# Kernel tuning notes

Measured on AMD Instinct MI355X. Metric: run time of the kernel, lower is better.

## Reference

```python
import jax, jax.numpy as jnp
import numpy as np

N_NODES = 100000
N_EDGES = 3200000
D_NODE = 5            # per-node feature dim
D_IN = 2 * D_NODE     # 10, MLP input dim
D_HID = D_IN * 5      # 50, HIDDEN_DIM_MULTIPLIER = 5


def setup_inputs() -> dict:
    key = jax.random.key(0)
    ks = jax.random.split(key, 8)
    x = jax.random.normal(ks[0], (N_NODES, D_NODE), dtype=jnp.float32)
    edge_index = jax.random.randint(ks[1], (2, N_EDGES), 0, N_NODES, dtype=jnp.int64)
    s1 = 1.0 / np.sqrt(D_IN)
    s2 = 1.0 / np.sqrt(D_HID)
    W1 = jax.random.uniform(ks[2], (D_IN, D_HID), jnp.float32, -s1, s1)
    b1 = jax.random.uniform(ks[3], (D_HID,), jnp.float32, -s1, s1)
    W2 = jax.random.uniform(ks[4], (D_HID, D_HID), jnp.float32, -s2, s2)
    b2 = jax.random.uniform(ks[5], (D_HID,), jnp.float32, -s2, s2)
    W3 = jax.random.uniform(ks[6], (D_HID, 1), jnp.float32, -s2, s2)
    b3 = jax.random.uniform(ks[7], (1,), jnp.float32, -s2, s2)
    return {"x": x, "edge_index": edge_index, "W1": W1, "b1": b1,
            "W2": W2, "b2": b2, "W3": W3, "b3": b3}


def reference(x, edge_index, W1, b1, W2, b2, W3, b3):
    # gather src/tgt node features and concat -> [E, 2*D_NODE]
    ef = jnp.concatenate([x[edge_index[0]], x[edge_index[1]]], axis=-1)
    h = jax.nn.relu(ef @ W1 + b1)
    h = jax.nn.relu(h @ W2 + b2)
    return jax.nn.sigmoid(h @ W3 + b3)  # [E, 1]
```

## Files before the change

### kernel.cpp

```cpp
#include <hip/hip_runtime.h>
#include <hip/hip_bf16.h>

typedef short bf16x8 __attribute__((ext_vector_type(8)));
typedef float f32x4  __attribute__((ext_vector_type(4)));

union fragU { f32x4 f; bf16x8 b; uint4 q; uint u[4]; };

__device__ inline ushort f2bf(float f) {
    union { float f; uint u; } v; v.f = f;
    uint r = (v.u + 0x7FFFu + ((v.u >> 16) & 1u)) >> 16;
    return (ushort)r;
}
__device__ inline uint packbf(float a, float b) {
    return (uint)f2bf(a) | ((uint)f2bf(b) << 16);
}
__device__ inline uint cvtpk(float lo, float hi) {
    uint r;
    asm("v_cvt_pk_bf16_f32 %0, %1, %2" : "=v"(r) : "v"(lo), "v"(hi));
    return r;
}

__global__ __launch_bounds__(256) void pack_x_kernel(
    const float* __restrict__ x, uint4* __restrict__ xp, int N)
{
    int i = blockIdx.x * blockDim.x + threadIdx.x;
    if (i > N) return;
    uint4 o = {0u, 0u, 0u, 0u};
    if (i < N) {
        const float* r = x + (size_t)i * 5;
        o.x = packbf(r[0], r[1]);
        o.y = packbf(r[2], r[3]);
        o.z = packbf(r[4], 1.0f);
    }
    xp[i] = o;
}

__global__ __launch_bounds__(64) void pack_w_kernel(
    const float* __restrict__ W1, const float* __restrict__ b1,
    const float* __restrict__ W2, const float* __restrict__ b2,
    const float* __restrict__ W3, uint4* __restrict__ tab)
{
    const int lane = threadIdx.x;
    const int c = lane & 15;
    const int g = lane >> 4;

    union { ushort s[8]; uint4 q; } u;
    #pragma unroll
    for (int mt = 0; mt < 4; ++mt) {
        #pragma unroll
        for (int d = 0; d < 8; ++d) {
            int k = 8 * g + d;
            int j = 16 * mt + c;
            float v = 0.f;
            if (j < 50) {
                if (k < 5)                 v = W1[k * 50 + j];
                else if (k == 5)           v = b1[j];
                else if (k >= 8 && k < 13) v = W1[(k - 3) * 50 + j];
            } else if (j == 50 && k == 5)  v = 1.0f;
            u.s[d] = f2bf(v);
        }
        tab[mt * 64 + lane] = u.q;
    }
    #pragma unroll
    for (int t = 0; t < 2; ++t) {
        #pragma unroll
        for (int mt = 0; mt < 4; ++mt) {
            #pragma unroll
            for (int d = 0; d < 8; ++d) {
                int hid1 = 16 * (2 * t + (d >> 2)) + 4 * g + (d & 3);
                int j    = 16 * mt + c;
                float v = 0.f;
                if (j < 50) {
                    if (hid1 < 50)       v = W2[hid1 * 50 + j];
                    else if (hid1 == 50) v = b2[j];
                }
                u.s[d] = f2bf(v);
            }
            tab[(4 + t * 4 + mt) * 64 + lane] = u.q;
        }
    }
    #pragma unroll
    for (int t = 0; t < 2; ++t) {
        #pragma unroll
        for (int d = 0; d < 8; ++d) {
            int hid = 16 * (2 * t + (d >> 2)) + 4 * g + (d & 3);
            float v = (c == 0 && hid < 50) ? W3[hid] : 0.f;
            u.s[d] = f2bf(v);
        }
        tab[(12 + t) * 64 + lane] = u.q;
    }
}

__global__ __launch_bounds__(256, 3) void edge_mlp_mfma6(
    const uint4* __restrict__ xp,
    const uint4* __restrict__ wtab,
    const int* __restrict__ ei,
    const float* __restrict__ b3,
    float* __restrict__ out, int E, int N, int num_tiles)
{
    const int tid  = threadIdx.x;
    const int w    = tid >> 6;
    const int lane = tid & 63;
    const int c    = lane & 15;
    const int g    = lane >> 4;

    fragU w1f[4], w2f[8], w3f[2];
    #pragma unroll
    for (int i = 0; i < 4; ++i) w1f[i].q = wtab[i * 64 + lane];
    #pragma unroll
    for (int i = 0; i < 8; ++i) w2f[i].q = wtab[(4 + i) * 64 + lane];
    #pragma unroll
    for (int i = 0; i < 2; ++i) w3f[i].q = wtab[(12 + i) * 64 + lane];

    asm volatile("" :
        "+v"(w1f[0].f), "+v"(w1f[1].f), "+v"(w1f[2].f), "+v"(w1f[3].f),
        "+v"(w2f[0].f), "+v"(w2f[1].f), "+v"(w2f[2].f), "+v"(w2f[3].f),
        "+v"(w2f[4].f), "+v"(w2f[5].f), "+v"(w2f[6].f), "+v"(w2f[7].f),
        "+v"(w3f[0].f), "+v"(w3f[1].f));

    const float b3s = b3[0];

    auto LOADF = [&](int bt_, fragU* a) {
        const int e0 = bt_ * 128 + w * 32;
        #pragma unroll
        for (int ms = 0; ms < 2; ++ms) {
            uint4 q = {0u, 0u, 0u, 0u};
            if (g < 2) {
                int e  = e0 + ms * 16 + c;
                int ee = (e < E) ? e : 0;
                int idx = ei[(size_t)g * (size_t)E + (size_t)ee];
                q = xp[idx];
            }
            a[ms].q = q;
        }
    };

    int bt = blockIdx.x;
    if (bt >= num_tiles) return;

    fragU aN[2];
    LOADF(bt, aN);

    for (; bt < num_tiles; bt += gridDim.x) {
        fragU aC[2];
        aC[0] = aN[0];
        aC[1] = aN[1];
        const int btn = bt + gridDim.x;
        if (btn < num_tiles) LOADF(btn, aN);

        const int e0 = bt * 128 + w * 32;

        #pragma unroll
        for (int ms = 0; ms < 2; ++ms) {
            f32x4 hT[4];
            #pragma unroll
            for (int mt = 0; mt < 4; ++mt) {
                f32x4 z = {0.f, 0.f, 0.f, 0.f};
                hT[mt] = __builtin_amdgcn_mfma_f32_16x16x32_bf16(w1f[mt].b, aC[ms].b, z, 0, 0, 0);
            }
            fragU bB0, bB1;
            #pragma unroll
            for (int mt = 0; mt < 2; ++mt) {
                bB0.u[2*mt]   = cvtpk(fmaxf(hT[mt][0], 0.f), fmaxf(hT[mt][1], 0.f));
                bB0.u[2*mt+1] = cvtpk(fmaxf(hT[mt][2], 0.f), fmaxf(hT[mt][3], 0.f));
                bB1.u[2*mt]   = cvtpk(fmaxf(hT[2+mt][0], 0.f), fmaxf(hT[2+mt][1], 0.f));
                bB1.u[2*mt+1] = cvtpk(fmaxf(hT[2+mt][2], 0.f), fmaxf(hT[2+mt][3], 0.f));
            }

            f32x4 h2T[4];
            #pragma unroll
            for (int mt = 0; mt < 4; ++mt) {
                f32x4 z = {0.f, 0.f, 0.f, 0.f};
                h2T[mt] = __builtin_amdgcn_mfma_f32_16x16x32_bf16(w2f[mt].b,     bB0.b, z, 0, 0, 0);
                h2T[mt] = __builtin_amdgcn_mfma_f32_16x16x32_bf16(w2f[4 + mt].b, bB1.b, h2T[mt], 0, 0, 0);
            }
            fragU cB0, cB1;
            #pragma unroll
            for (int mt = 0; mt < 2; ++mt) {
                cB0.u[2*mt]   = cvtpk(fmaxf(h2T[mt][0], 0.f), fmaxf(h2T[mt][1], 0.f));
                cB0.u[2*mt+1] = cvtpk(fmaxf(h2T[mt][2], 0.f), fmaxf(h2T[mt][3], 0.f));
                cB1.u[2*mt]   = cvtpk(fmaxf(h2T[2+mt][0], 0.f), fmaxf(h2T[2+mt][1], 0.f));
                cB1.u[2*mt+1] = cvtpk(fmaxf(h2T[2+mt][2], 0.f), fmaxf(h2T[2+mt][3], 0.f));
            }

            f32x4 z3 = {0.f, 0.f, 0.f, 0.f};
            f32x4 o3 = __builtin_amdgcn_mfma_f32_16x16x32_bf16(w3f[0].b, cB0.b, z3, 0, 0, 0);
            o3 = __builtin_amdgcn_mfma_f32_16x16x32_bf16(w3f[1].b, cB1.b, o3, 0, 0, 0);

            if (g == 0) {
                int e = e0 + ms * 16 + c;
                if (e < E) {
                    float zz = o3[0] + b3s;
                    out[e] = 1.f / (1.f + __expf(-zz));
                }
            }
        }
    }
}

extern "C" void kernel_launch(void* const* d_in, const int* in_sizes, int n_in,
                              void* d_out, int out_size, void* d_ws, size_t ws_size,
                              hipStream_t stream) {
    const float* x  = (const float*)d_in[0];
    const int*   ei = (const int*)d_in[1];
    const float* W1 = (const float*)d_in[2];
    const float* b1 = (const float*)d_in[3];
    const float* W2 = (const float*)d_in[4];
    const float* b2 = (const float*)d_in[5];
    const float* W3 = (const float*)d_in[6];
    const float* b3 = (const float*)d_in[7];
    float* out = (float*)d_out;

    int E = in_sizes[1] / 2;
    int N = in_sizes[0] / 5;

    uint4* wtab = (uint4*)d_ws;
    uint4* xp   = (uint4*)((char*)d_ws + 16384);

    pack_w_kernel<<<1, 64, 0, stream>>>(W1, b1, W2, b2, W3, wtab);
    pack_x_kernel<<<(N + 1 + 255) / 256, 256, 0, stream>>>(x, xp, N);

    int num_tiles = (E + 127) / 128;
    int grid = num_tiles < 2048 ? num_tiles : 2048;
    edge_mlp_mfma6<<<grid, 256, 0, stream>>>(xp, wtab, ei, b3, out, E, N, num_tiles);
}
```

Measured before the change: 76.76 us.

## Stage weights in LDS and pipeline index loads two tiles ahead

Weights move from per-lane registers into a shared-memory table loaded once per block, and each MFMA reads its fragment from LDS. This frees VGPRs so launch bounds can rise from 3 to 4 blocks per SIMD. The prefetch is split into two stages: edge indices are loaded two tiles ahead and node gathers one tile ahead, to hide the dependent global-load latency. The trade-off is extra LDS reads on every tile and more in-flight registers for the prefetch; the sigmoid also uses a fast reciprocal.

```diff
diff --git a/kernel.cpp b/kernel.cpp
--- a/kernel.cpp
+++ b/kernel.cpp
@@ -91,110 +91,116 @@
     }
 }
 
-__global__ __launch_bounds__(256, 3) void edge_mlp_mfma6(
+__global__ __launch_bounds__(256, 4) void edge_mlp_mfma7(
     const uint4* __restrict__ xp,
     const uint4* __restrict__ wtab,
     const int* __restrict__ ei,
     const float* __restrict__ b3,
     float* __restrict__ out, int E, int N, int num_tiles)
 {
-    const int tid  = threadIdx.x;
+    __shared__ uint4 lds_w[896];
+
+    const int tid = threadIdx.x;
+    #pragma unroll
+    for (int i = 0; i < 4; ++i) lds_w[tid + 256 * i] = wtab[tid + 256 * i];
+    if (tid < 896 - 1024 + 256) {  }
+    if (tid < 128) lds_w[768 + tid] = wtab[768 + tid];
+    __syncthreads();
+
     const int w    = tid >> 6;
     const int lane = tid & 63;
     const int c    = lane & 15;
     const int g    = lane >> 4;
-
-    fragU w1f[4], w2f[8], w3f[2];
-    #pragma unroll
-    for (int i = 0; i < 4; ++i) w1f[i].q = wtab[i * 64 + lane];
-    #pragma unroll
-    for (int i = 0; i < 8; ++i) w2f[i].q = wtab[(4 + i) * 64 + lane];
-    #pragma unroll
-    for (int i = 0; i < 2; ++i) w3f[i].q = wtab[(12 + i) * 64 + lane];
-
-    asm volatile("" :
-        "+v"(w1f[0].f), "+v"(w1f[1].f), "+v"(w1f[2].f), "+v"(w1f[3].f),
-        "+v"(w2f[0].f), "+v"(w2f[1].f), "+v"(w2f[2].f), "+v"(w2f[3].f),
-        "+v"(w2f[4].f), "+v"(w2f[5].f), "+v"(w2f[6].f), "+v"(w2f[7].f),
-        "+v"(w3f[0].f), "+v"(w3f[1].f));
+    const int G    = gridDim.x;
 
     const float b3s = b3[0];
 
-    auto LOADF = [&](int bt_, fragU* a) {
-        const int e0 = bt_ * 128 + w * 32;
-        #pragma unroll
-        for (int ms = 0; ms < 2; ++ms) {
-            uint4 q = {0u, 0u, 0u, 0u};
-            if (g < 2) {
-                int e  = e0 + ms * 16 + c;
-                int ee = (e < E) ? e : 0;
-                int idx = ei[(size_t)g * (size_t)E + (size_t)ee];
-                q = xp[idx];
-            }
-            a[ms].q = q;
+    auto LOAD_IDX = [&](int bt_) -> int2 {
+        int bc = (bt_ < num_tiles) ? bt_ : (num_tiles - 1);
+        int2 r; r.x = 0; r.y = 0;
+        if (g < 2) {
+            const int e0 = bc * 128 + w * 32;
+            int eA = e0 + c;      if (eA >= E) eA = 0;
+            int eB = e0 + 16 + c; if (eB >= E) eB = 0;
+            const int* row = ei + (size_t)g * (size_t)E;
+            r.x = row[eA];
+            r.y = row[eB];
+        }
+        return r;
+    };
+    auto GATHER = [&](int2 idx, fragU* a) {
+        uint4 q0 = {0u,0u,0u,0u}, q1 = {0u,0u,0u,0u};
+        if (g < 2) { q0 = xp[idx.x]; q1 = xp[idx.y]; }
+        a[0].q = q0; a[1].q = q1;
+    };
+
+    auto COMP = [&](fragU aX, int e) {
+        f32x4 hT[4];
+        #pragma unroll
+        for (int mt = 0; mt < 4; ++mt) {
+            fragU w1; w1.q = lds_w[mt * 64 + lane];
+            f32x4 z = {0.f, 0.f, 0.f, 0.f};
+            hT[mt] = __builtin_amdgcn_mfma_f32_16x16x32_bf16(w1.b, aX.b, z, 0, 0, 0);
+        }
+        fragU bB0, bB1;
+        #pragma unroll
+        for (int mt = 0; mt < 2; ++mt) {
+            bB0.u[2*mt]   = cvtpk(fmaxf(hT[mt][0], 0.f),   fmaxf(hT[mt][1], 0.f));
+            bB0.u[2*mt+1] = cvtpk(fmaxf(hT[mt][2], 0.f),   fmaxf(hT[mt][3], 0.f));
+            bB1.u[2*mt]   = cvtpk(fmaxf(hT[2+mt][0], 0.f), fmaxf(hT[2+mt][1], 0.f));
+            bB1.u[2*mt+1] = cvtpk(fmaxf(hT[2+mt][2], 0.f), fmaxf(hT[2+mt][3], 0.f));
+        }
+        f32x4 h2T[4];
+        #pragma unroll
+        for (int mt = 0; mt < 4; ++mt) {
+            fragU wa, wb;
+            wa.q = lds_w[(4 + mt) * 64 + lane];
+            wb.q = lds_w[(8 + mt) * 64 + lane];
+            f32x4 z = {0.f, 0.f, 0.f, 0.f};
+            h2T[mt] = __builtin_amdgcn_mfma_f32_16x16x32_bf16(wa.b, bB0.b, z, 0, 0, 0);
+            h2T[mt] = __builtin_amdgcn_mfma_f32_16x16x32_bf16(wb.b, bB1.b, h2T[mt], 0, 0, 0);
+        }
+        fragU cB0, cB1;
+        #pragma unroll
+        for (int mt = 0; mt < 2; ++mt) {
+            cB0.u[2*mt]   = cvtpk(fmaxf(h2T[mt][0], 0.f),   fmaxf(h2T[mt][1], 0.f));
+            cB0.u[2*mt+1] = cvtpk(fmaxf(h2T[mt][2], 0.f),   fmaxf(h2T[mt][3], 0.f));
+            cB1.u[2*mt]   = cvtpk(fmaxf(h2T[2+mt][0], 0.f), fmaxf(h2T[2+mt][1], 0.f));
+            cB1.u[2*mt+1] = cvtpk(fmaxf(h2T[2+mt][2], 0.f), fmaxf(h2T[2+mt][3], 0.f));
+        }
+        fragU w3a, w3b;
+        w3a.q = lds_w[12 * 64 + lane];
+        w3b.q = lds_w[13 * 64 + lane];
+        f32x4 z3 = {0.f, 0.f, 0.f, 0.f};
+        f32x4 o3 = __builtin_amdgcn_mfma_f32_16x16x32_bf16(w3a.b, cB0.b, z3, 0, 0, 0);
+        o3 = __builtin_amdgcn_mfma_f32_16x16x32_bf16(w3b.b, cB1.b, o3, 0, 0, 0);
+
+        if (g == 0 && e < E) {
+            float zz = o3[0] + b3s;
+            float ex = __expf(-zz);
+            out[e] = __builtin_amdgcn_rcpf(1.f + ex);
         }
     };
 
     int bt = blockIdx.x;
     if (bt >= num_tiles) return;
 
-    fragU aN[2];
-    LOADF(bt, aN);
-
-    for (; bt < num_tiles; bt += gridDim.x) {
-        fragU aC[2];
-        aC[0] = aN[0];
-        aC[1] = aN[1];
-        const int btn = bt + gridDim.x;
-        if (btn < num_tiles) LOADF(btn, aN);
+    int2 idxC = LOAD_IDX(bt);
+    fragU fC[2];
+    GATHER(idxC, fC);
+    int2 idxN = LOAD_IDX(bt + G);
+
+    for (; bt < num_tiles; bt += G) {
+        fragU fN[2];
+        GATHER(idxN, fN);
+        idxN = LOAD_IDX(bt + 2 * G);
 
         const int e0 = bt * 128 + w * 32;
-
-        #pragma unroll
-        for (int ms = 0; ms < 2; ++ms) {
-            f32x4 hT[4];
-            #pragma unroll
-            for (int mt = 0; mt < 4; ++mt) {
-                f32x4 z = {0.f, 0.f, 0.f, 0.f};
-                hT[mt] = __builtin_amdgcn_mfma_f32_16x16x32_bf16(w1f[mt].b, aC[ms].b, z, 0, 0, 0);
-            }
-            fragU bB0, bB1;
-            #pragma unroll
-            for (int mt = 0; mt < 2; ++mt) {
-                bB0.u[2*mt]   = cvtpk(fmaxf(hT[mt][0], 0.f), fmaxf(hT[mt][1], 0.f));
-                bB0.u[2*mt+1] = cvtpk(fmaxf(hT[mt][2], 0.f), fmaxf(hT[mt][3], 0.f));
-                bB1.u[2*mt]   = cvtpk(fmaxf(hT[2+mt][0], 0.f), fmaxf(hT[2+mt][1], 0.f));
-                bB1.u[2*mt+1] = cvtpk(fmaxf(hT[2+mt][2], 0.f), fmaxf(hT[2+mt][3], 0.f));
-            }
-
-            f32x4 h2T[4];
-            #pragma unroll
-            for (int mt = 0; mt < 4; ++mt) {
-                f32x4 z = {0.f, 0.f, 0.f, 0.f};
-                h2T[mt] = __builtin_amdgcn_mfma_f32_16x16x32_bf16(w2f[mt].b,     bB0.b, z, 0, 0, 0);
-                h2T[mt] = __builtin_amdgcn_mfma_f32_16x16x32_bf16(w2f[4 + mt].b, bB1.b, h2T[mt], 0, 0, 0);
-            }
-            fragU cB0, cB1;
-            #pragma unroll
-            for (int mt = 0; mt < 2; ++mt) {
-                cB0.u[2*mt]   = cvtpk(fmaxf(h2T[mt][0], 0.f), fmaxf(h2T[mt][1], 0.f));
-                cB0.u[2*mt+1] = cvtpk(fmaxf(h2T[mt][2], 0.f), fmaxf(h2T[mt][3], 0.f));
-                cB1.u[2*mt]   = cvtpk(fmaxf(h2T[2+mt][0], 0.f), fmaxf(h2T[2+mt][1], 0.f));
-                cB1.u[2*mt+1] = cvtpk(fmaxf(h2T[2+mt][2], 0.f), fmaxf(h2T[2+mt][3], 0.f));
-            }
-
-            f32x4 z3 = {0.f, 0.f, 0.f, 0.f};
-            f32x4 o3 = __builtin_amdgcn_mfma_f32_16x16x32_bf16(w3f[0].b, cB0.b, z3, 0, 0, 0);
-            o3 = __builtin_amdgcn_mfma_f32_16x16x32_bf16(w3f[1].b, cB1.b, o3, 0, 0, 0);
-
-            if (g == 0) {
-                int e = e0 + ms * 16 + c;
-                if (e < E) {
-                    float zz = o3[0] + b3s;
-                    out[e] = 1.f / (1.f + __expf(-zz));
-                }
-            }
-        }
+        COMP(fC[0], e0 + c);
+        COMP(fC[1], e0 + 16 + c);
+
+        fC[0] = fN[0];
+        fC[1] = fN[1];
     }
 }
 
@@ -222,5 +228,5 @@
 
     int num_tiles = (E + 127) / 128;
     int grid = num_tiles < 2048 ? num_tiles : 2048;
-    edge_mlp_mfma6<<<grid, 256, 0, stream>>>(xp, wtab, ei, b3, out, E, N, num_tiles);
-}
+    edge_mlp_mfma7<<<grid, 256, 0, stream>>>(xp, wtab, ei, b3, out, E, N, num_tiles);
+}
```

Measured after the change: 70.59 us. 8.0% less time.

## Double tile size, split index and gather prefetch into two-stage pipeline

Applied to the files above, without the earlier changes.

Each block tile now covers 256 edges (64 per wave), and two independent 16-edge streams are interleaved through the MFMA chain to hide MFMA dependency latency. Edge-index loads are prefetched two tiles ahead and node-feature gathers one tile ahead, which splits the dependent index->gather load chain across iterations. The sigmoid uses a hardware reciprocal. This raises register pressure (more fragments in flight) under the 3-blocks-per-SM launch bound, and there are half as many tiles for the same grid cap.

```diff
diff --git a/kernel.cpp b/kernel.cpp
--- a/kernel.cpp
+++ b/kernel.cpp
@@ -91,18 +91,19 @@
     }
 }
 
-__global__ __launch_bounds__(256, 3) void edge_mlp_mfma6(
+__global__ __launch_bounds__(256, 3) void edge_mlp_mfma8(
     const uint4* __restrict__ xp,
     const uint4* __restrict__ wtab,
     const int* __restrict__ ei,
     const float* __restrict__ b3,
-    float* __restrict__ out, int E, int N, int num_tiles)
+    float* __restrict__ out, int E, int num_tiles)
 {
     const int tid  = threadIdx.x;
     const int w    = tid >> 6;
     const int lane = tid & 63;
     const int c    = lane & 15;
     const int g    = lane >> 4;
+    const int G    = gridDim.x;
 
     fragU w1f[4], w2f[8], w3f[2];
     #pragma unroll
@@ -111,7 +112,6 @@
     for (int i = 0; i < 8; ++i) w2f[i].q = wtab[(4 + i) * 64 + lane];
     #pragma unroll
     for (int i = 0; i < 2; ++i) w3f[i].q = wtab[(12 + i) * 64 + lane];
-
     asm volatile("" :
         "+v"(w1f[0].f), "+v"(w1f[1].f), "+v"(w1f[2].f), "+v"(w1f[3].f),
         "+v"(w2f[0].f), "+v"(w2f[1].f), "+v"(w2f[2].f), "+v"(w2f[3].f),
@@ -120,17 +120,25 @@
 
     const float b3s = b3[0];
 
-    auto LOADF = [&](int bt_, fragU* a) {
-        const int e0 = bt_ * 128 + w * 32;
-        #pragma unroll
-        for (int ms = 0; ms < 2; ++ms) {
+    auto LOAD_IDX = [&](int bt_, int* id) {
+        int bc = (bt_ < num_tiles) ? bt_ : (num_tiles - 1);
+        const int e0 = bc * 256 + w * 64;
+        #pragma unroll
+        for (int ms = 0; ms < 4; ++ms) {
+            int v = 0;
+            if (g < 2) {
+                int e = e0 + ms * 16 + c;
+                if (e >= E) e = 0;
+                v = ei[(size_t)g * (size_t)E + (size_t)e];
+            }
+            id[ms] = v;
+        }
+    };
+    auto GATHER = [&](const int* id, fragU* a) {
+        #pragma unroll
+        for (int ms = 0; ms < 4; ++ms) {
             uint4 q = {0u, 0u, 0u, 0u};
-            if (g < 2) {
-                int e  = e0 + ms * 16 + c;
-                int ee = (e < E) ? e : 0;
-                int idx = ei[(size_t)g * (size_t)E + (size_t)ee];
-                q = xp[idx];
-            }
+            if (g < 2) q = xp[id[ms]];
             a[ms].q = q;
         }
     };
@@ -138,63 +146,90 @@
     int bt = blockIdx.x;
     if (bt >= num_tiles) return;
 
-    fragU aN[2];
-    LOADF(bt, aN);
-
-    for (; bt < num_tiles; bt += gridDim.x) {
-        fragU aC[2];
-        aC[0] = aN[0];
-        aC[1] = aN[1];
-        const int btn = bt + gridDim.x;
-        if (btn < num_tiles) LOADF(btn, aN);
-
-        const int e0 = bt * 128 + w * 32;
-
-        #pragma unroll
-        for (int ms = 0; ms < 2; ++ms) {
-            f32x4 hT[4];
+    fragU fC[4], fN[4];
+    int idxN[4];
+    {
+        int id0[4];
+        LOAD_IDX(bt, id0);
+        GATHER(id0, fC);
+    }
+    LOAD_IDX(bt + G, idxN);
+
+    for (; bt < num_tiles; bt += G) {
+        GATHER(idxN, fN);
+        LOAD_IDX(bt + 2 * G, idxN);
+
+        const int e0 = bt * 256 + w * 64;
+
+        #pragma unroll
+        for (int half = 0; half < 2; ++half) {
+            const fragU aA = fC[2 * half];
+            const fragU aB = fC[2 * half + 1];
+
+            f32x4 hA[4], hB[4];
             #pragma unroll
             for (int mt = 0; mt < 4; ++mt) {
                 f32x4 z = {0.f, 0.f, 0.f, 0.f};
-                hT[mt] = __builtin_amdgcn_mfma_f32_16x16x32_bf16(w1f[mt].b, aC[ms].b, z, 0, 0, 0);
-            }
-            fragU bB0, bB1;
+                hA[mt] = __builtin_amdgcn_mfma_f32_16x16x32_bf16(w1f[mt].b, aA.b, z, 0, 0, 0);
+                hB[mt] = __builtin_amdgcn_mfma_f32_16x16x32_bf16(w1f[mt].b, aB.b, z, 0, 0, 0);
+            }
+            fragU bA0, bA1, bB0, bB1;
             #pragma unroll
             for (int mt = 0; mt < 2; ++mt) {
-                bB0.u[2*mt]   = cvtpk(fmaxf(hT[mt][0], 0.f), fmaxf(hT[mt][1], 0.f));
-                bB0.u[2*mt+1] = cvtpk(fmaxf(hT[mt][2], 0.f), fmaxf(hT[mt][3], 0.f));
-                bB1.u[2*mt]   = cvtpk(fmaxf(hT[2+mt][0], 0.f), fmaxf(hT[2+mt][1], 0.f));
-                bB1.u[2*mt+1] = cvtpk(fmaxf(hT[2+mt][2], 0.f), fmaxf(hT[2+mt][3], 0.f));
-            }
-
-            f32x4 h2T[4];
+                bA0.u[2*mt]   = cvtpk(fmaxf(hA[mt][0], 0.f),   fmaxf(hA[mt][1], 0.f));
+                bA0.u[2*mt+1] = cvtpk(fmaxf(hA[mt][2], 0.f),   fmaxf(hA[mt][3], 0.f));
+                bA1.u[2*mt]   = cvtpk(fmaxf(hA[2+mt][0], 0.f), fmaxf(hA[2+mt][1], 0.f));
+                bA1.u[2*mt+1] = cvtpk(fmaxf(hA[2+mt][2], 0.f), fmaxf(hA[2+mt][3], 0.f));
+                bB0.u[2*mt]   = cvtpk(fmaxf(hB[mt][0], 0.f),   fmaxf(hB[mt][1], 0.f));
+                bB0.u[2*mt+1] = cvtpk(fmaxf(hB[mt][2], 0.f),   fmaxf(hB[mt][3], 0.f));
+                bB1.u[2*mt]   = cvtpk(fmaxf(hB[2+mt][0], 0.f), fmaxf(hB[2+mt][1], 0.f));
+                bB1.u[2*mt+1] = cvtpk(fmaxf(hB[2+mt][2], 0.f), fmaxf(hB[2+mt][3], 0.f));
+            }
+
+            f32x4 h2A[4], h2B[4];
             #pragma unroll
             for (int mt = 0; mt < 4; ++mt) {
                 f32x4 z = {0.f, 0.f, 0.f, 0.f};
-                h2T[mt] = __builtin_amdgcn_mfma_f32_16x16x32_bf16(w2f[mt].b,     bB0.b, z, 0, 0, 0);
-                h2T[mt] = __builtin_amdgcn_mfma_f32_16x16x32_bf16(w2f[4 + mt].b, bB1.b, h2T[mt], 0, 0, 0);
-            }
-            fragU cB0, cB1;
+                h2A[mt] = __builtin_amdgcn_mfma_f32_16x16x32_bf16(w2f[mt].b,     bA0.b, z, 0, 0, 0);
+                h2B[mt] = __builtin_amdgcn_mfma_f32_16x16x32_bf16(w2f[mt].b,     bB0.b, z, 0, 0, 0);
+                h2A[mt] = __builtin_amdgcn_mfma_f32_16x16x32_bf16(w2f[4 + mt].b, bA1.b, h2A[mt], 0, 0, 0);
+                h2B[mt] = __builtin_amdgcn_mfma_f32_16x16x32_bf16(w2f[4 + mt].b, bB1.b, h2B[mt], 0, 0, 0);
+            }
+            fragU cA0, cA1, cB0, cB1;
             #pragma unroll
             for (int mt = 0; mt < 2; ++mt) {
-                cB0.u[2*mt]   = cvtpk(fmaxf(h2T[mt][0], 0.f), fmaxf(h2T[mt][1], 0.f));
-                cB0.u[2*mt+1] = cvtpk(fmaxf(h2T[mt][2], 0.f), fmaxf(h2T[mt][3], 0.f));
-                cB1.u[2*mt]   = cvtpk(fmaxf(h2T[2+mt][0], 0.f), fmaxf(h2T[2+mt][1], 0.f));
-                cB1.u[2*mt+1] = cvtpk(fmaxf(h2T[2+mt][2], 0.f), fmaxf(h2T[2+mt][3], 0.f));
+                cA0.u[2*mt]   = cvtpk(fmaxf(h2A[mt][0], 0.f),   fmaxf(h2A[mt][1], 0.f));
+                cA0.u[2*mt+1] = cvtpk(fmaxf(h2A[mt][2], 0.f),   fmaxf(h2A[mt][3], 0.f));
+                cA1.u[2*mt]   = cvtpk(fmaxf(h2A[2+mt][0], 0.f), fmaxf(h2A[2+mt][1], 0.f));
+                cA1.u[2*mt+1] = cvtpk(fmaxf(h2A[2+mt][2], 0.f), fmaxf(h2A[2+mt][3], 0.f));
+                cB0.u[2*mt]   = cvtpk(fmaxf(h2B[mt][0], 0.f),   fmaxf(h2B[mt][1], 0.f));
+                cB0.u[2*mt+1] = cvtpk(fmaxf(h2B[mt][2], 0.f),   fmaxf(h2B[mt][3], 0.f));
+                cB1.u[2*mt]   = cvtpk(fmaxf(h2B[2+mt][0], 0.f), fmaxf(h2B[2+mt][1], 0.f));
+                cB1.u[2*mt+1] = cvtpk(fmaxf(h2B[2+mt][2], 0.f), fmaxf(h2B[2+mt][3], 0.f));
             }
 
             f32x4 z3 = {0.f, 0.f, 0.f, 0.f};
-            f32x4 o3 = __builtin_amdgcn_mfma_f32_16x16x32_bf16(w3f[0].b, cB0.b, z3, 0, 0, 0);
-            o3 = __builtin_amdgcn_mfma_f32_16x16x32_bf16(w3f[1].b, cB1.b, o3, 0, 0, 0);
+            f32x4 oA = __builtin_amdgcn_mfma_f32_16x16x32_bf16(w3f[0].b, cA0.b, z3, 0, 0, 0);
+            f32x4 oB = __builtin_amdgcn_mfma_f32_16x16x32_bf16(w3f[0].b, cB0.b, z3, 0, 0, 0);
+            oA = __builtin_amdgcn_mfma_f32_16x16x32_bf16(w3f[1].b, cA1.b, oA, 0, 0, 0);
+            oB = __builtin_amdgcn_mfma_f32_16x16x32_bf16(w3f[1].b, cB1.b, oB, 0, 0, 0);
 
             if (g == 0) {
-                int e = e0 + ms * 16 + c;
-                if (e < E) {
-                    float zz = o3[0] + b3s;
-                    out[e] = 1.f / (1.f + __expf(-zz));
+                int eA = e0 + (2 * half) * 16 + c;
+                int eB = eA + 16;
+                if (eA < E) {
+                    float ex = __expf(-(oA[0] + b3s));
+                    out[eA] = __builtin_amdgcn_rcpf(1.f + ex);
                 }
-            }
-        }
+                if (eB < E) {
+                    float ex = __expf(-(oB[0] + b3s));
+                    out[eB] = __builtin_amdgcn_rcpf(1.f + ex);
+                }
+            }
+        }
+
+        #pragma unroll
+        for (int i = 0; i < 4; ++i) fC[i] = fN[i];
     }
 }
 
@@ -220,7 +255,7 @@
     pack_w_kernel<<<1, 64, 0, stream>>>(W1, b1, W2, b2, W3, wtab);
     pack_x_kernel<<<(N + 1 + 255) / 256, 256, 0, stream>>>(x, xp, N);
 
-    int num_tiles = (E + 127) / 128;
+    int num_tiles = (E + 255) / 256;
     int grid = num_tiles < 2048 ? num_tiles : 2048;
-    edge_mlp_mfma6<<<grid, 256, 0, stream>>>(xp, wtab, ei, b3, out, E, N, num_tiles);
-}
+    edge_mlp_mfma8<<<grid, 256, 0, stream>>>(xp, wtab, ei, b3, out, E, num_tiles);
+}
```

Result: no change. 76.61 us (-0.2%).

## Two-stage software pipeline splitting index loads from gathers with smaller tiles

Applied to the files above, without the earlier changes.

Shrinks the tile to 64 edges per block (16 per wave) and restructures prefetching into two stages: edge indices are loaded two iterations ahead and node features are gathered one iteration ahead. This aims to hide the dependent index-then-gather latency chain. Occupancy hint raised from 3 to 4 blocks per CU, and the sigmoid divide is replaced by a hardware reciprocal. The risks are more loop iterations and register pressure under the tighter bound, plus a small loss of precision in the sigmoid.

```diff
diff --git a/kernel.cpp b/kernel.cpp
--- a/kernel.cpp
+++ b/kernel.cpp
@@ -91,18 +91,19 @@
     }
 }
 
-__global__ __launch_bounds__(256, 3) void edge_mlp_mfma6(
+__global__ __launch_bounds__(256, 4) void edge_mlp_mfma9(
     const uint4* __restrict__ xp,
     const uint4* __restrict__ wtab,
     const int* __restrict__ ei,
     const float* __restrict__ b3,
-    float* __restrict__ out, int E, int N, int num_tiles)
+    float* __restrict__ out, int E, int num_tiles)
 {
     const int tid  = threadIdx.x;
     const int w    = tid >> 6;
     const int lane = tid & 63;
     const int c    = lane & 15;
     const int g    = lane >> 4;
+    const int G    = gridDim.x;
 
     fragU w1f[4], w2f[8], w3f[2];
     #pragma unroll
@@ -111,7 +112,6 @@
     for (int i = 0; i < 8; ++i) w2f[i].q = wtab[(4 + i) * 64 + lane];
     #pragma unroll
     for (int i = 0; i < 2; ++i) w3f[i].q = wtab[(12 + i) * 64 + lane];
-
     asm volatile("" :
         "+v"(w1f[0].f), "+v"(w1f[1].f), "+v"(w1f[2].f), "+v"(w1f[3].f),
         "+v"(w2f[0].f), "+v"(w2f[1].f), "+v"(w2f[2].f), "+v"(w2f[3].f),
@@ -120,81 +120,78 @@
 
     const float b3s = b3[0];
 
-    auto LOADF = [&](int bt_, fragU* a) {
-        const int e0 = bt_ * 128 + w * 32;
-        #pragma unroll
-        for (int ms = 0; ms < 2; ++ms) {
-            uint4 q = {0u, 0u, 0u, 0u};
-            if (g < 2) {
-                int e  = e0 + ms * 16 + c;
-                int ee = (e < E) ? e : 0;
-                int idx = ei[(size_t)g * (size_t)E + (size_t)ee];
-                q = xp[idx];
-            }
-            a[ms].q = q;
-        }
+    auto LOAD_IDX = [&](int bt_) -> int {
+        int bc = (bt_ < num_tiles) ? bt_ : (num_tiles - 1);
+        int v = 0;
+        if (g < 2) {
+            int e = bc * 64 + w * 16 + c;
+            if (e >= E) e = 0;
+            v = ei[(size_t)g * (size_t)E + (size_t)e];
+        }
+        return v;
+    };
+    auto GATHER = [&](int idx) -> fragU {
+        fragU a;
+        uint4 q = {0u, 0u, 0u, 0u};
+        if (g < 2) q = xp[idx];
+        a.q = q;
+        return a;
     };
 
     int bt = blockIdx.x;
     if (bt >= num_tiles) return;
 
-    fragU aN[2];
-    LOADF(bt, aN);
-
-    for (; bt < num_tiles; bt += gridDim.x) {
-        fragU aC[2];
-        aC[0] = aN[0];
-        aC[1] = aN[1];
-        const int btn = bt + gridDim.x;
-        if (btn < num_tiles) LOADF(btn, aN);
-
-        const int e0 = bt * 128 + w * 32;
-
-        #pragma unroll
-        for (int ms = 0; ms < 2; ++ms) {
-            f32x4 hT[4];
-            #pragma unroll
-            for (int mt = 0; mt < 4; ++mt) {
-                f32x4 z = {0.f, 0.f, 0.f, 0.f};
-                hT[mt] = __builtin_amdgcn_mfma_f32_16x16x32_bf16(w1f[mt].b, aC[ms].b, z, 0, 0, 0);
+    fragU fC = GATHER(LOAD_IDX(bt));
+    int idxN = LOAD_IDX(bt + G);
+
+    for (; bt < num_tiles; bt += G) {
+        fragU fN = GATHER(idxN);
+        idxN = LOAD_IDX(bt + 2 * G);
+
+        f32x4 hT[4];
+        #pragma unroll
+        for (int mt = 0; mt < 4; ++mt) {
+            f32x4 z = {0.f, 0.f, 0.f, 0.f};
+            hT[mt] = __builtin_amdgcn_mfma_f32_16x16x32_bf16(w1f[mt].b, fC.b, z, 0, 0, 0);
+        }
+        fragU bB0, bB1;
+        #pragma unroll
+        for (int mt = 0; mt < 2; ++mt) {
+            bB0.u[2*mt]   = cvtpk(fmaxf(hT[mt][0], 0.f),   fmaxf(hT[mt][1], 0.f));
+            bB0.u[2*mt+1] = cvtpk(fmaxf(hT[mt][2], 0.f),   fmaxf(hT[mt][3], 0.f));
+            bB1.u[2*mt]   = cvtpk(fmaxf(hT[2+mt][0], 0.f), fmaxf(hT[2+mt][1], 0.f));
+            bB1.u[2*mt+1] = cvtpk(fmaxf(hT[2+mt][2], 0.f), fmaxf(hT[2+mt][3], 0.f));
+        }
+
+        f32x4 h2T[4];
+        #pragma unroll
+        for (int mt = 0; mt < 4; ++mt) {
+            f32x4 z = {0.f, 0.f, 0.f, 0.f};
+            h2T[mt] = __builtin_amdgcn_mfma_f32_16x16x32_bf16(w2f[mt].b,     bB0.b, z, 0, 0, 0);
+            h2T[mt] = __builtin_amdgcn_mfma_f32_16x16x32_bf16(w2f[4 + mt].b, bB1.b, h2T[mt], 0, 0, 0);
+        }
+        fragU cB0, cB1;
+        #pragma unroll
+        for (int mt = 0; mt < 2; ++mt) {
+            cB0.u[2*mt]   = cvtpk(fmaxf(h2T[mt][0], 0.f),   fmaxf(h2T[mt][1], 0.f));
+            cB0.u[2*mt+1] = cvtpk(fmaxf(h2T[mt][2], 0.f),   fmaxf(h2T[mt][3], 0.f));
+            cB1.u[2*mt]   = cvtpk(fmaxf(h2T[2+mt][0], 0.f), fmaxf(h2T[2+mt][1], 0.f));
+            cB1.u[2*mt+1] = cvtpk(fmaxf(h2T[2+mt][2], 0.f), fmaxf(h2T[2+mt][3], 0.f));
+        }
+
+        f32x4 z3 = {0.f, 0.f, 0.f, 0.f};
+        f32x4 o3 = __builtin_amdgcn_mfma_f32_16x16x32_bf16(w3f[0].b, cB0.b, z3, 0, 0, 0);
+        o3 = __builtin_amdgcn_mfma_f32_16x16x32_bf16(w3f[1].b, cB1.b, o3, 0, 0, 0);
+
+        if (g == 0) {
+            int e = bt * 64 + w * 16 + c;
+            if (e < E) {
+                float ex = __expf(-(o3[0] + b3s));
+                out[e] = __builtin_amdgcn_rcpf(1.f + ex);
             }
-            fragU bB0, bB1;
-            #pragma unroll
-            for (int mt = 0; mt < 2; ++mt) {
-                bB0.u[2*mt]   = cvtpk(fmaxf(hT[mt][0], 0.f), fmaxf(hT[mt][1], 0.f));
-                bB0.u[2*mt+1] = cvtpk(fmaxf(hT[mt][2], 0.f), fmaxf(hT[mt][3], 0.f));
-                bB1.u[2*mt]   = cvtpk(fmaxf(hT[2+mt][0], 0.f), fmaxf(hT[2+mt][1], 0.f));
-                bB1.u[2*mt+1] = cvtpk(fmaxf(hT[2+mt][2], 0.f), fmaxf(hT[2+mt][3], 0.f));
-            }
-
-            f32x4 h2T[4];
-            #pragma unroll
-            for (int mt = 0; mt < 4; ++mt) {
-                f32x4 z = {0.f, 0.f, 0.f, 0.f};
-                h2T[mt] = __builtin_amdgcn_mfma_f32_16x16x32_bf16(w2f[mt].b,     bB0.b, z, 0, 0, 0);
-                h2T[mt] = __builtin_amdgcn_mfma_f32_16x16x32_bf16(w2f[4 + mt].b, bB1.b, h2T[mt], 0, 0, 0);
-            }
-            fragU cB0, cB1;
-            #pragma unroll
-            for (int mt = 0; mt < 2; ++mt) {
-                cB0.u[2*mt]   = cvtpk(fmaxf(h2T[mt][0], 0.f), fmaxf(h2T[mt][1], 0.f));
-                cB0.u[2*mt+1] = cvtpk(fmaxf(h2T[mt][2], 0.f), fmaxf(h2T[mt][3], 0.f));
-                cB1.u[2*mt]   = cvtpk(fmaxf(h2T[2+mt][0], 0.f), fmaxf(h2T[2+mt][1], 0.f));
-                cB1.u[2*mt+1] = cvtpk(fmaxf(h2T[2+mt][2], 0.f), fmaxf(h2T[2+mt][3], 0.f));
-            }
-
-            f32x4 z3 = {0.f, 0.f, 0.f, 0.f};
-            f32x4 o3 = __builtin_amdgcn_mfma_f32_16x16x32_bf16(w3f[0].b, cB0.b, z3, 0, 0, 0);
-            o3 = __builtin_amdgcn_mfma_f32_16x16x32_bf16(w3f[1].b, cB1.b, o3, 0, 0, 0);
-
-            if (g == 0) {
-                int e = e0 + ms * 16 + c;
-                if (e < E) {
-                    float zz = o3[0] + b3s;
-                    out[e] = 1.f / (1.f + __expf(-zz));
-                }
-            }
-        }
+        }
+
+        fC = fN;
     }
 }
 
@@ -220,7 +217,7 @@
     pack_w_kernel<<<1, 64, 0, stream>>>(W1, b1, W2, b2, W3, wtab);
     pack_x_kernel<<<(N + 1 + 255) / 256, 256, 0, stream>>>(x, xp, N);
 
-    int num_tiles = (E + 127) / 128;
+    int num_tiles = (E + 63) / 64;
     int grid = num_tiles < 2048 ? num_tiles : 2048;
-    edge_mlp_mfma6<<<grid, 256, 0, stream>>>(xp, wtab, ei, b3, out, E, N, num_tiles);
-}
+    edge_mlp_mfma9<<<grid, 256, 0, stream>>>(xp, wtab, ei, b3, out, E, num_tiles);
+}
```

Measured after the change: 77.29 us. No clear change (+0.7%).
